# Optimization experiments

Hardware: AMD Instinct MI355X
Metric: run time of the kernel (lower is better)

Reference implementation:

```python
import jax, jax.numpy as jnp
import numpy as np
import math

D_EMB = 1024
N_HEADS = 16
D_HEAD = D_EMB // N_HEADS
D_FF = 4 * D_EMB
BATCH = 2
SEQ = 2048
EPS = 1e-6


def setup_inputs() -> dict:
    key = jax.random.key(0)
    ks = jax.random.split(key, 12)
    s = 0.02
    return {
        "x": jax.random.normal(ks[0], (BATCH, SEQ, D_EMB), jnp.float32),
        "wq": jax.random.normal(ks[1], (D_EMB, D_EMB), jnp.float32) * s,
        "wk": jax.random.normal(ks[2], (D_EMB, D_EMB), jnp.float32) * s,
        "wv": jax.random.normal(ks[3], (D_EMB, D_EMB), jnp.float32) * s,
        "wo": jax.random.normal(ks[4], (D_EMB, D_EMB), jnp.float32) * s,
        "bo": jnp.zeros((D_EMB,), jnp.float32),
        "w1": jax.random.normal(ks[5], (D_FF, D_EMB), jnp.float32) * s,
        "b1": jnp.zeros((D_FF,), jnp.float32),
        "w2": jax.random.normal(ks[6], (D_EMB, D_FF), jnp.float32) * s,
        "b2": jnp.zeros((D_EMB,), jnp.float32),
        "ln1_s": jnp.ones((D_EMB,), jnp.float32),
        "ln1_b": jnp.zeros((D_EMB,), jnp.float32),
        "ln2_s": jnp.ones((D_EMB,), jnp.float32),
        "ln2_b": jnp.zeros((D_EMB,), jnp.float32),
    }


def _layernorm(x, scale, shift):
    mean = jnp.mean(x, axis=-1, keepdims=True)
    var = jnp.mean(jnp.square(x - mean), axis=-1, keepdims=True)  # unbiased=False
    return scale * (x - mean) / jnp.sqrt(var + EPS) + shift


def _gelu_tanh(x):
    c = math.sqrt(2.0 / math.pi)
    return 0.5 * x * (1.0 + jnp.tanh(c * (x + 0.044715 * x * x * x)))


def _attention(x, wq, wk, wv, wo, bo):
    B, S, _ = x.shape
    q = (x @ wq.T).reshape(B, S, N_HEADS, D_HEAD).transpose(0, 2, 1, 3)
    k = (x @ wk.T).reshape(B, S, N_HEADS, D_HEAD).transpose(0, 2, 1, 3)
    v = (x @ wv.T).reshape(B, S, N_HEADS, D_HEAD).transpose(0, 2, 1, 3)
    scores = jnp.einsum("bhqd,bhkd->bhqk", q, k)
    causal = jnp.triu(jnp.ones((S, S), bool), k=1)
    scores = jnp.where(causal, -jnp.inf, scores)
    weights = jax.nn.softmax(scores / math.sqrt(D_HEAD), axis=-1)
    ctx = jnp.einsum("bhqk,bhkd->bhqd", weights, v)
    ctx = ctx.transpose(0, 2, 1, 3).reshape(B, S, D_EMB)
    return ctx @ wo.T + bo


def reference(x, wq, wk, wv, wo, bo, w1, b1, w2, b2, ln1_s, ln1_b, ln2_s, ln2_b):
    # pre-norm attention block (dropout in eval mode = identity)
    h = x + _attention(_layernorm(x, ln1_s, ln1_b), wq, wk, wv, wo, bo)
    # pre-norm MLP with tanh-approx GeLU
    y = _layernorm(h, ln2_s, ln2_b)
    y = _gelu_tanh(y @ w1.T + b1) @ w2.T + b2
    return h + y
```

## Files before the change

kernel.cpp:

```cpp
#include <hip/hip_runtime.h>
#include <math.h>

typedef unsigned short u16;
typedef __attribute__((ext_vector_type(8))) __bf16 bf16x8v;
typedef __attribute__((ext_vector_type(8))) unsigned short ushort8v;
typedef __attribute__((ext_vector_type(4))) unsigned short ushort4v;
typedef __attribute__((ext_vector_type(4))) float f32x4v;

#define D_EMBD 1024
#define NHEADS 16
#define DHEAD  64
#define DFF    4096
#define BATCHN 2
#define SEQL   2048
#define TOK    (BATCHN*SEQL)

#define EPI_BF16_GELU    2
#define EPI_BF16_QKV     3
#define EPI_BF16_PART    5

__device__ __forceinline__ float bf2f(u16 s) {
  return __builtin_bit_cast(float, (unsigned)s << 16);
}
__device__ __forceinline__ u16 f2bf(float f) {
  unsigned u = __builtin_bit_cast(unsigned, f);
  unsigned r = u + 0x7fffu + ((u >> 16) & 1u);
  return (u16)(r >> 16);
}
__device__ __forceinline__ u16 f2bf_trunc(float f) {
  return (u16)(__builtin_bit_cast(unsigned, f) >> 16);
}

#define GLOAD16(gp, lp)                                                        \
  __builtin_amdgcn_global_load_lds(                                            \
      (__attribute__((address_space(1))) void*)(void*)(gp),                    \
      (__attribute__((address_space(3))) void*)(void*)(lp), 16, 0, 0)

__global__ __launch_bounds__(256) void cvt_all_kernel(const float* __restrict__ wq,
                                                      const float* __restrict__ wk,
                                                      const float* __restrict__ wv,
                                                      const float* __restrict__ wo,
                                                      const float* __restrict__ w1,
                                                      const float* __restrict__ w2,
                                                      u16* __restrict__ wcat,
                                                      u16* __restrict__ wob,
                                                      u16* __restrict__ w1b,
                                                      u16* __restrict__ w2b) {
  int bid = blockIdx.x;
  const float* src;
  u16* dst;
  int loc;
  if (bid < 4096) {
    int seg = bid >> 10;
    loc = (bid & 1023) * 256 + threadIdx.x;
    src = (seg == 0) ? wq : (seg == 1) ? wk : (seg == 2) ? wv : wo;
    dst = (seg == 0) ? wcat : (seg == 1) ? wcat + 1048576
                            : (seg == 2) ? wcat + 2097152 : wob;
  } else if (bid < 8192) {
    loc = (bid - 4096) * 256 + threadIdx.x;
    src = w1; dst = w1b;
  } else {
    loc = (bid - 8192) * 256 + threadIdx.x;
    src = w2; dst = w2b;
  }
  float4 v = ((const float4*)src)[loc];
  ushort4 o;
  o.x = f2bf(v.x); o.y = f2bf(v.y); o.z = f2bf(v.z); o.w = f2bf(v.w);
  ((ushort4*)dst)[loc] = o;
}

__global__ __launch_bounds__(256) void ln_kernel(const float* __restrict__ x,
                                                 const float* __restrict__ sc,
                                                 const float* __restrict__ sh,
                                                 u16* __restrict__ out) {
  int row = blockIdx.x, tid = threadIdx.x;
  const float4* xr = (const float4*)(x + (size_t)row * D_EMBD);
  float4 v = xr[tid];
  float s  = (v.x + v.y) + (v.z + v.w);
  float s2 = (v.x * v.x + v.y * v.y) + (v.z * v.z + v.w * v.w);
#pragma unroll
  for (int off = 32; off; off >>= 1) {
    s  += __shfl_xor(s, off, 64);
    s2 += __shfl_xor(s2, off, 64);
  }
  __shared__ float rs[4], rs2[4];
  int wave = tid >> 6, lane = tid & 63;
  if (lane == 0) { rs[wave] = s; rs2[wave] = s2; }
  __syncthreads();
  s  = (rs[0] + rs[1]) + (rs[2] + rs[3]);
  s2 = (rs2[0] + rs2[1]) + (rs2[2] + rs2[3]);
  float mean = s * (1.f / 1024.f);
  float var  = s2 * (1.f / 1024.f) - mean * mean;
  float rstd = rsqrtf(var + 1e-6f);
  float4 scv = ((const float4*)sc)[tid];
  float4 shv = ((const float4*)sh)[tid];
  ushort4 o;
  o.x = f2bf((v.x - mean) * rstd * scv.x + shv.x);
  o.y = f2bf((v.y - mean) * rstd * scv.y + shv.y);
  o.z = f2bf((v.z - mean) * rstd * scv.z + shv.z);
  o.w = f2bf((v.w - mean) * rstd * scv.w + shv.w);
  ((ushort4*)(out + (size_t)row * D_EMBD))[tid] = o;
}

__global__ __launch_bounds__(256) void ln2f_kernel(const u16* __restrict__ parts,
                                                   const float* __restrict__ x,
                                                   const float* __restrict__ bo,
                                                   const float* __restrict__ sc,
                                                   const float* __restrict__ sh,
                                                   float* __restrict__ hbuf,
                                                   u16* __restrict__ ybuf) {
  int row = blockIdx.x, tid = threadIdx.x;
  size_t base4 = (size_t)row * 256 + tid;
  float4 v = ((const float4*)x)[base4];
  float4 bv = ((const float4*)bo)[tid];
  v.x += bv.x; v.y += bv.y; v.z += bv.z; v.w += bv.w;
#pragma unroll
  for (int p = 0; p < 4; ++p) {
    ushort4 u = ((const ushort4*)parts)[(size_t)p * 1048576 + base4];
    v.x += bf2f(u.x); v.y += bf2f(u.y); v.z += bf2f(u.z); v.w += bf2f(u.w);
  }
  ((float4*)hbuf)[base4] = v;
  float s  = (v.x + v.y) + (v.z + v.w);
  float s2 = (v.x * v.x + v.y * v.y) + (v.z * v.z + v.w * v.w);
#pragma unroll
  for (int off = 32; off; off >>= 1) {
    s  += __shfl_xor(s, off, 64);
    s2 += __shfl_xor(s2, off, 64);
  }
  __shared__ float rs[4], rs2[4];
  int wave = tid >> 6, lane = tid & 63;
  if (lane == 0) { rs[wave] = s; rs2[wave] = s2; }
  __syncthreads();
  s  = (rs[0] + rs[1]) + (rs[2] + rs[3]);
  s2 = (rs2[0] + rs2[1]) + (rs2[2] + rs2[3]);
  float mean = s * (1.f / 1024.f);
  float var  = s2 * (1.f / 1024.f) - mean * mean;
  float rstd = rsqrtf(var + 1e-6f);
  float4 scv = ((const float4*)sc)[tid];
  float4 shv = ((const float4*)sh)[tid];
  ushort4 o;
  o.x = f2bf((v.x - mean) * rstd * scv.x + shv.x);
  o.y = f2bf((v.y - mean) * rstd * scv.y + shv.y);
  o.z = f2bf((v.z - mean) * rstd * scv.z + shv.z);
  o.w = f2bf((v.w - mean) * rstd * scv.w + shv.w);
  ((ushort4*)ybuf)[base4] = o;
}

__global__ __launch_bounds__(256) void reduce_w2_kernel(const u16* __restrict__ parts,
                                                        const float* __restrict__ resid,
                                                        const float* __restrict__ bias,
                                                        float* __restrict__ out) {
  int i = blockIdx.x * 256 + threadIdx.x;
  float4 r = ((const float4*)resid)[i];
  float4 bi = ((const float4*)bias)[i & 255];
  float s0 = 0, s1 = 0, s2 = 0, s3 = 0;
#pragma unroll
  for (int p = 0; p < 4; ++p) {
    ushort4 u = ((const ushort4*)parts)[(size_t)p * 1048576 + i];
    s0 += bf2f(u.x); s1 += bf2f(u.y); s2 += bf2f(u.z); s3 += bf2f(u.w);
  }
  float4 o = {s0 + r.x + bi.x, s1 + r.y + bi.y, s2 + r.z + bi.z, s3 + r.w + bi.w};
  ((float4*)out)[i] = o;
}

template <int MH, int NH, bool READA, class FS, class FG>
__device__ __forceinline__ void gphase(const u16* sm, int cur, int wm, int wn,
                                       int lr, int quad,
                                       f32x4v (&acc)[8][4], bf16x8v (&av)[4][2],
                                       FS&& st, FG&& gate) {
  const int sx = lr & 7;
  bf16x8v bv[2][2];
  if constexpr (READA) {
#pragma unroll
    for (int j2 = 0; j2 < 4; ++j2) {
      int g = 2 * (MH * 4 + j2) + wm;
      int row = g * 16 + lr;
#pragma unroll
      for (int kk = 0; kk < 2; ++kk) {
        int slot = (kk * 4 + quad) ^ sx;
        av[j2][kk] = *(const bf16x8v*)(sm + cur * 32768 + row * 64 + slot * 8);
      }
    }
  }
#pragma unroll
  for (int i2 = 0; i2 < 2; ++i2) {
    int h = wn + 4 * (NH * 2 + i2);
    int row = h * 16 + lr;
#pragma unroll
    for (int kk = 0; kk < 2; ++kk) {
      int slot = (kk * 4 + quad) ^ sx;
      bv[i2][kk] = *(const bf16x8v*)(sm + cur * 32768 + 16384 + row * 64 + slot * 8);
    }
  }
  st();
  gate();
  __builtin_amdgcn_s_barrier();
  asm volatile("s_waitcnt lgkmcnt(0)" ::: "memory");
  __builtin_amdgcn_sched_barrier(0);
  __builtin_amdgcn_s_setprio(1);
#pragma unroll
  for (int j2 = 0; j2 < 4; ++j2)
#pragma unroll
    for (int i2 = 0; i2 < 2; ++i2)
#pragma unroll
      for (int kk = 0; kk < 2; ++kk)
        acc[MH * 4 + j2][NH * 2 + i2] = __builtin_amdgcn_mfma_f32_16x16x32_bf16(
            av[j2][kk], bv[i2][kk], acc[MH * 4 + j2][NH * 2 + i2], 0, 0, 0);
  __builtin_amdgcn_s_setprio(0);
  __builtin_amdgcn_sched_barrier(0);
  __builtin_amdgcn_s_barrier();
}

template <int EPI>
__global__ __launch_bounds__(512, 2) void gemm256(const u16* __restrict__ A,
                                                  const u16* __restrict__ W,
                                                  u16* __restrict__ Cb,
                                                  const float* __restrict__ bias,
                                                  int M, int N, int K) {
  __shared__ __align__(16) u16 sm[65536];
  const int tid = threadIdx.x;
  const int wave = tid >> 6, lane = tid & 63;
  const int lr = lane & 15, quad = lane >> 4;
  const int wm = wave >> 2, wn = wave & 3;
  const int m0 = blockIdx.y * 256, n0 = blockIdx.x * 256;
  const int KC = K / gridDim.z;
  const int kbeg = blockIdx.z * KC;
  const int NT = KC >> 6;
  const size_t poff = (size_t)blockIdx.z * ((size_t)M * N);

  const int r8 = lane >> 3;
  const int sslot = (lane & 7) ^ r8;
  const int rb0 = wave * 2;

  auto stA = [&](int bb, int h, int tk) {
#pragma unroll
    for (int s = 0; s < 2; ++s) {
      const u16* gp = A + (size_t)(m0 + h * 128 + (rb0 + s) * 8 + r8) * K +
                      (kbeg + tk * 64 + sslot * 8);
      GLOAD16(gp, (char*)sm + bb * 65536 + h * 16384 + (rb0 + s) * 1024);
    }
  };
  auto stB = [&](int bb, int h, int tk) {
#pragma unroll
    for (int s = 0; s < 2; ++s) {
      const u16* gp = W + (size_t)(n0 + h * 128 + (rb0 + s) * 8 + r8) * K +
                      (kbeg + tk * 64 + sslot * 8);
      GLOAD16(gp, (char*)sm + bb * 65536 + 32768 + h * 16384 + (rb0 + s) * 1024);
    }
  };

  f32x4v acc[8][4];
#pragma unroll
  for (int j = 0; j < 8; ++j)
#pragma unroll
    for (int i = 0; i < 4; ++i) {
      f32x4v z = {0.f, 0.f, 0.f, 0.f};
      acc[j][i] = z;
    }
  bf16x8v av[4][2];

  stA(0, 0, 0); stB(0, 0, 0); stA(0, 1, 0); stB(0, 1, 0);
  stA(1, 0, 1); stB(1, 1, 1);
  asm volatile("s_waitcnt vmcnt(4)" ::: "memory");
  __builtin_amdgcn_s_barrier();

  for (int t = 0; t < NT; ++t) {
    const int cur = t & 1, nb = cur ^ 1;
    const bool p1 = (t + 1 < NT), p2 = (t + 2 < NT);
    gphase<0, 0, true>(sm, cur, wm, wn, lr, quad, acc, av,
        [&] { if (p1) stB(nb, 0, t + 1); }, [&] {});
    gphase<0, 1, false>(sm, cur, wm, wn, lr, quad, acc, av,
        [&] { if (p1) stA(nb, 1, t + 1); }, [&] {});
    gphase<1, 1, true>(sm, cur, wm, wn, lr, quad, acc, av,
        [&] { if (p2) stA(cur, 0, t + 2); }, [&] {});
    gphase<1, 0, false>(sm, cur, wm, wn, lr, quad, acc, av,
        [&] { if (p2) stB(cur, 1, t + 2); },
        [&] {
          if (p2) { asm volatile("s_waitcnt vmcnt(4)" ::: "memory"); }
          else    { asm volatile("s_waitcnt vmcnt(0)" ::: "memory"); }
        });
  }

  const bool qsc = (EPI == EPI_BF16_QKV) && (n0 < 1024);
#pragma unroll
  for (int j = 0; j < 8; ++j) {
    int gr = m0 + (2 * j + wm) * 16 + quad * 4;
#pragma unroll
    for (int i = 0; i < 4; ++i) {
      int gc = n0 + (wn + 4 * i) * 16 + lr;
      float bi = 0.f;
      if constexpr (EPI == EPI_BF16_GELU) bi = bias[gc];
#pragma unroll
      for (int r = 0; r < 4; ++r) {
        size_t idx = (size_t)(gr + r) * N + gc;
        float v = acc[j][i][r];
        if constexpr (EPI == EPI_BF16_PART) {
          Cb[poff + idx] = f2bf(v);
        } else if constexpr (EPI == EPI_BF16_QKV) {
          Cb[idx] = f2bf(qsc ? v * 0.125f : v);
        } else {
          v += bi;
          float z = 0.7978845608028654f * (v + 0.044715f * v * v * v);
          float tt = 2.f / (1.f + __expf(-2.f * z)) - 1.f;
          Cb[idx] = f2bf(0.5f * v * (1.f + tt));
        }
      }
    }
  }
}

#define VTS 72
__device__ __forceinline__ void stage_k8(const u16* Kbase, int ks, u16* kfbuf,
                                         int wave, int lr, int quad) {
  int key = ((wave >> 1) << 4) + lr;
  int c8 = ((wave & 1) << 2) + quad;
  GLOAD16(Kbase + (size_t)(ks + key) * 3072 + c8 * 8, (char*)kfbuf + wave * 1024);
}
__device__ __forceinline__ void load_v(const u16* Vbase, int ks, int vkey0, int vc8,
                                       ushort8v& va, ushort8v& vb) {
  va = *(const ushort8v*)(Vbase + (size_t)(ks + vkey0) * 3072 + vc8 * 8);
  vb = *(const ushort8v*)(Vbase + (size_t)(ks + vkey0 + 1) * 3072 + vc8 * 8);
}
__device__ __forceinline__ void write_vt(u16* vt, int vc8, int vcol,
                                         ushort8v va, ushort8v vb) {
#pragma unroll
  for (int j = 0; j < 8; ++j) {
    unsigned pk = (unsigned)va[j] | ((unsigned)vb[j] << 16);
    *(unsigned*)(vt + (size_t)(vc8 * 8 + j) * VTS + vcol) = pk;
  }
}

__global__ __launch_bounds__(512) void attn_kernel(const u16* __restrict__ qkv,
                                                   u16* __restrict__ ctx) {
  __shared__ u16 Kf[2][4096];
  __shared__ u16 Vt[2][64 * VTS];
  int tid = threadIdx.x;
  int wave = tid >> 6, lane = tid & 63;
  int lr = lane & 15, quad = lane >> 4;
  int id = blockIdx.x;
  int bh = id & 31;
  int t = 15 - (id >> 5);
  int b = bh >> 4, h = bh & 15;
  int q0 = t * 128;
  const u16* qkvb = qkv + (size_t)(b * SEQL) * 3072;
  int qrow = q0 + wave * 16 + lr;
  const u16* Qp = qkvb + (size_t)qrow * 3072 + h * 64 + quad * 8;
  bf16x8v qf0 = *(const bf16x8v*)(Qp);
  bf16x8v qf1 = *(const bf16x8v*)(Qp + 32);
  const u16* Kbase = qkvb + 1024 + h * 64;
  const u16* Vbase = qkvb + 2048 + h * 64;
  const bool vstager = (tid < 256);
  int vkey0 = ((tid & 255) >> 3) * 2, vc8 = tid & 7;
  int vcol = vkey0 ^ (vc8 << 2);

  float m = -INFINITY, l = 0.f;
  f32x4v accO[4];
#pragma unroll
  for (int r = 0; r < 4; r++) {
    f32x4v z = {0.f, 0.f, 0.f, 0.f};
    accO[r] = z;
  }

  int nkt = 2 * t + 2;
  {
    stage_k8(Kbase, 0, Kf[0], wave, lr, quad);
    if (vstager) {
      ushort8v va, vb;
      load_v(Vbase, 0, vkey0, vc8, va, vb);
      write_vt(Vt[0], vc8, vcol, va, vb);
    }
  }
  __syncthreads();

  for (int kt = 0; kt < nkt; ++kt) {
    int cur = kt & 1, nxt = cur ^ 1;
    ushort8v va, vb;
    bool pre = (kt + 1 < nkt);
    if (pre) {
      stage_k8(Kbase, (kt + 1) * 64, Kf[nxt], wave, lr, quad);
      if (vstager) load_v(Vbase, (kt + 1) * 64, vkey0, vc8, va, vb);
    }
    bool active = !(kt == 2 * t + 1 && wave < 4);
    if (active) {
      const bf16x8v* Kc = (const bf16x8v*)Kf[cur];
      const u16* Vc = Vt[cur];
      f32x4v accS[4];
#pragma unroll
      for (int jb = 0; jb < 4; jb++) {
        f32x4v z = {0.f, 0.f, 0.f, 0.f};
        accS[jb] = z;
      }
#pragma unroll
      for (int jb = 0; jb < 4; jb++) {
        accS[jb] = __builtin_amdgcn_mfma_f32_16x16x32_bf16(Kc[((jb * 2 + 0) << 6) + lane], qf0, accS[jb], 0, 0, 0);
        accS[jb] = __builtin_amdgcn_mfma_f32_16x16x32_bf16(Kc[((jb * 2 + 1) << 6) + lane], qf1, accS[jb], 0, 0, 0);
      }
      if (kt >= 2 * t) {
        int kb = (kt - 2 * t) << 6;
#pragma unroll
        for (int jb = 0; jb < 4; jb++)
#pragma unroll
          for (int r = 0; r < 4; r++)
            if (kb + jb * 16 + quad * 4 + r > wave * 16 + lr) accS[jb][r] = -INFINITY;
      }
      float smax = accS[0][0];
#pragma unroll
      for (int jb = 0; jb < 4; jb++)
#pragma unroll
        for (int r = 0; r < 4; r++) smax = fmaxf(smax, accS[jb][r]);
      smax = fmaxf(smax, __shfl_xor(smax, 16, 64));
      smax = fmaxf(smax, __shfl_xor(smax, 32, 64));
      float mn = fmaxf(m, smax);
      float alpha = __expf(m - mn);
      m = mn;
      float ps = 0.f;
#pragma unroll
      for (int jb = 0; jb < 4; jb++)
#pragma unroll
        for (int r = 0; r < 4; r++) {
          accS[jb][r] = __expf(accS[jb][r] - mn);
          ps += accS[jb][r];
        }
      ps += __shfl_xor(ps, 16, 64);
      ps += __shfl_xor(ps, 32, 64);
      l = l * alpha + ps;
      float ar[4];
#pragma unroll
      for (int r = 0; r < 4; r++) ar[r] = __shfl(alpha, quad * 4 + r, 16);
#pragma unroll
      for (int nb = 0; nb < 4; nb++)
#pragma unroll
        for (int r = 0; r < 4; r++) accO[nb][r] *= ar[r];
#pragma unroll
      for (int kk = 0; kk < 2; ++kk) {
        ushort8v pp;
#pragma unroll
        for (int j = 0; j < 4; ++j) {
          pp[j]     = f2bf_trunc(accS[2 * kk][j]);
          pp[j + 4] = f2bf_trunc(accS[2 * kk + 1][j]);
        }
        bf16x8v pav = __builtin_bit_cast(bf16x8v, pp);
#pragma unroll
        for (int nb = 0; nb < 4; nb++) {
          int dim = nb * 16 + lr;
          int f = (nb * 2 + (lr >> 3)) & 7;
          int col1 = (kk * 32 + quad * 4) ^ (f << 2);
          ushort4v v0 = *(const ushort4v*)(Vc + dim * VTS + col1);
          ushort4v v1 = *(const ushort4v*)(Vc + dim * VTS + (col1 ^ 16));
          ushort8v vv;
#pragma unroll
          for (int j = 0; j < 4; ++j) { vv[j] = v0[j]; vv[j + 4] = v1[j]; }
          accO[nb] = __builtin_amdgcn_mfma_f32_16x16x32_bf16(pav, __builtin_bit_cast(bf16x8v, vv), accO[nb], 0, 0, 0);
        }
      }
    }
    if (pre && vstager) write_vt(Vt[nxt], vc8, vcol, va, vb);
    __syncthreads();
  }
  float linv = 1.f / l;
  float rr[4];
#pragma unroll
  for (int r = 0; r < 4; r++) rr[r] = __shfl(linv, quad * 4 + r, 16);
#pragma unroll
  for (int nb = 0; nb < 4; nb++)
#pragma unroll
    for (int r = 0; r < 4; r++) {
      int rowg = q0 + wave * 16 + quad * 4 + r;
      ctx[(size_t)(b * SEQL + rowg) * D_EMBD + h * 64 + nb * 16 + lr] =
          f2bf(accO[nb][r] * rr[r]);
    }
}

extern "C" void kernel_launch(void* const* d_in, const int* in_sizes, int n_in,
                              void* d_out, int out_size, void* d_ws, size_t ws_size,
                              hipStream_t stream) {
  const float* x    = (const float*)d_in[0];
  const float* wq   = (const float*)d_in[1];
  const float* wk   = (const float*)d_in[2];
  const float* wv   = (const float*)d_in[3];
  const float* wo   = (const float*)d_in[4];
  const float* bo   = (const float*)d_in[5];
  const float* w1   = (const float*)d_in[6];
  const float* b1   = (const float*)d_in[7];
  const float* w2   = (const float*)d_in[8];
  const float* b2   = (const float*)d_in[9];
  const float* ln1s = (const float*)d_in[10];
  const float* ln1b = (const float*)d_in[11];
  const float* ln2s = (const float*)d_in[12];
  const float* ln2b = (const float*)d_in[13];
  float* out = (float*)d_out;

  char* base = (char*)d_ws;
  size_t off = 0;
  auto alloc = [&](size_t bytes) {
    char* r = base + off;
    off += (bytes + 255) & ~(size_t)255;
    return r;
  };
  u16*   wcat = (u16*)alloc((size_t)3072 * 1024 * 2);
  u16*   wob  = (u16*)alloc((size_t)1024 * 1024 * 2);
  u16*   w1b  = (u16*)alloc((size_t)4096 * 1024 * 2);
  u16*   w2b  = (u16*)alloc((size_t)1024 * 4096 * 2);
  u16*   xn   = (u16*)alloc((size_t)TOK * 1024 * 2);
  u16*   qkv  = (u16*)alloc((size_t)TOK * 3072 * 2);
  u16*   ctx  = (u16*)alloc((size_t)TOK * 1024 * 2);
  float* hbuf = (float*)alloc((size_t)TOK * 1024 * 4);
  u16*   ybuf = (u16*)alloc((size_t)TOK * 1024 * 2);
  u16*   gbuf = (u16*)alloc((size_t)TOK * 4096 * 2);
  u16* woP = (u16*)xn;
  u16* w2P = (u16*)xn;

  cvt_all_kernel<<<12288, 256, 0, stream>>>(wq, wk, wv, wo, w1, w2,
                                            wcat, wob, w1b, w2b);
  ln_kernel<<<TOK, 256, 0, stream>>>(x, ln1s, ln1b, xn);
  gemm256<EPI_BF16_QKV><<<dim3(12, 16), 512, 0, stream>>>(
      xn, wcat, qkv, nullptr, TOK, 3072, 1024);
  attn_kernel<<<512, 512, 0, stream>>>(qkv, ctx);
  gemm256<EPI_BF16_PART><<<dim3(4, 16, 4), 512, 0, stream>>>(
      ctx, wob, woP, nullptr, TOK, 1024, 1024);
  ln2f_kernel<<<TOK, 256, 0, stream>>>(woP, x, bo, ln2s, ln2b, hbuf, ybuf);
  gemm256<EPI_BF16_GELU><<<dim3(16, 16), 512, 0, stream>>>(
      ybuf, w1b, gbuf, b1, TOK, 4096, 1024);
  gemm256<EPI_BF16_PART><<<dim3(4, 16, 4), 512, 0, stream>>>(
      gbuf, w2b, w2P, nullptr, TOK, 1024, 4096);
  reduce_w2_kernel<<<4096, 256, 0, stream>>>(w2P, hbuf, b2, out);
}
```

Baseline: 339.4 us.

## Swizzle GEMM block order across XCDs and reuse B fragments across phases

```diff
diff --git a/kernel.cpp b/kernel.cpp
--- a/kernel.cpp
+++ b/kernel.cpp
@@ -163,53 +163,9 @@
   ((float4*)out)[i] = o;
 }
 
-template <int MH, int NH, bool READA, class FS, class FG>
-__device__ __forceinline__ void gphase(const u16* sm, int cur, int wm, int wn,
-                                       int lr, int quad,
-                                       f32x4v (&acc)[8][4], bf16x8v (&av)[4][2],
-                                       FS&& st, FG&& gate) {
-  const int sx = lr & 7;
-  bf16x8v bv[2][2];
-  if constexpr (READA) {
-#pragma unroll
-    for (int j2 = 0; j2 < 4; ++j2) {
-      int g = 2 * (MH * 4 + j2) + wm;
-      int row = g * 16 + lr;
-#pragma unroll
-      for (int kk = 0; kk < 2; ++kk) {
-        int slot = (kk * 4 + quad) ^ sx;
-        av[j2][kk] = *(const bf16x8v*)(sm + cur * 32768 + row * 64 + slot * 8);
-      }
-    }
-  }
-#pragma unroll
-  for (int i2 = 0; i2 < 2; ++i2) {
-    int h = wn + 4 * (NH * 2 + i2);
-    int row = h * 16 + lr;
-#pragma unroll
-    for (int kk = 0; kk < 2; ++kk) {
-      int slot = (kk * 4 + quad) ^ sx;
-      bv[i2][kk] = *(const bf16x8v*)(sm + cur * 32768 + 16384 + row * 64 + slot * 8);
-    }
-  }
-  st();
-  gate();
-  __builtin_amdgcn_s_barrier();
-  asm volatile("s_waitcnt lgkmcnt(0)" ::: "memory");
-  __builtin_amdgcn_sched_barrier(0);
-  __builtin_amdgcn_s_setprio(1);
-#pragma unroll
-  for (int j2 = 0; j2 < 4; ++j2)
-#pragma unroll
-    for (int i2 = 0; i2 < 2; ++i2)
-#pragma unroll
-      for (int kk = 0; kk < 2; ++kk)
-        acc[MH * 4 + j2][NH * 2 + i2] = __builtin_amdgcn_mfma_f32_16x16x32_bf16(
-            av[j2][kk], bv[i2][kk], acc[MH * 4 + j2][NH * 2 + i2], 0, 0, 0);
-  __builtin_amdgcn_s_setprio(0);
-  __builtin_amdgcn_sched_barrier(0);
-  __builtin_amdgcn_s_barrier();
-}
+#define GBAR  __builtin_amdgcn_s_barrier()
+#define LGKM0 do { asm volatile("s_waitcnt lgkmcnt(0)" ::: "memory"); \
+                   __builtin_amdgcn_sched_barrier(0); } while (0)
 
 template <int EPI>
 __global__ __launch_bounds__(512, 2) void gemm256(const u16* __restrict__ A,
@@ -222,15 +178,23 @@
   const int wave = tid >> 6, lane = tid & 63;
   const int lr = lane & 15, quad = lane >> 4;
   const int wm = wave >> 2, wn = wave & 3;
-  const int m0 = blockIdx.y * 256, n0 = blockIdx.x * 256;
+  const int gx = gridDim.x, gy = gridDim.y;
+  const int nwg = gx * gy * gridDim.z;
+  const int bid = blockIdx.x + gx * (blockIdx.y + gy * blockIdx.z);
+  const int swz = (bid & 7) * (nwg >> 3) + (bid >> 3);
+  const int bx = swz % gx;
+  const int r1 = swz / gx;
+  const int by = r1 % gy, bz = r1 / gy;
+  const int m0 = by * 256, n0 = bx * 256;
   const int KC = K / gridDim.z;
-  const int kbeg = blockIdx.z * KC;
+  const int kbeg = bz * KC;
   const int NT = KC >> 6;
-  const size_t poff = (size_t)blockIdx.z * ((size_t)M * N);
+  const size_t poff = (size_t)bz * ((size_t)M * N);
 
   const int r8 = lane >> 3;
   const int sslot = (lane & 7) ^ r8;
   const int rb0 = wave * 2;
+  const int sx = lr & 7;
 
   auto stA = [&](int bb, int h, int tk) {
 #pragma unroll
@@ -248,6 +212,28 @@
       GLOAD16(gp, (char*)sm + bb * 65536 + 32768 + h * 16384 + (rb0 + s) * 1024);
     }
   };
+  auto ldA = [&](bf16x8v (&av)[4][2], int mh, int cur) {
+#pragma unroll
+    for (int j2 = 0; j2 < 4; ++j2) {
+      int row = (2 * (mh * 4 + j2) + wm) * 16 + lr;
+#pragma unroll
+      for (int kk = 0; kk < 2; ++kk) {
+        int slot = (kk * 4 + quad) ^ sx;
+        av[j2][kk] = *(const bf16x8v*)(sm + cur * 32768 + row * 64 + slot * 8);
+      }
+    }
+  };
+  auto ldB = [&](bf16x8v (&bv)[2][2], int nh, int cur) {
+#pragma unroll
+    for (int i2 = 0; i2 < 2; ++i2) {
+      int row = (wn + 4 * (nh * 2 + i2)) * 16 + lr;
+#pragma unroll
+      for (int kk = 0; kk < 2; ++kk) {
+        int slot = (kk * 4 + quad) ^ sx;
+        bv[i2][kk] = *(const bf16x8v*)(sm + cur * 32768 + 16384 + row * 64 + slot * 8);
+      }
+    }
+  };
 
   f32x4v acc[8][4];
 #pragma unroll
@@ -257,28 +243,46 @@
       f32x4v z = {0.f, 0.f, 0.f, 0.f};
       acc[j][i] = z;
     }
-  bf16x8v av[4][2];
+  bf16x8v av[4][2], bv0[2][2], bv1[2][2];
+
+  auto MMA = [&](int mh, int nh, bf16x8v (&a)[4][2], bf16x8v (&b)[2][2]) {
+    GBAR;
+    LGKM0;
+    __builtin_amdgcn_s_setprio(1);
+#pragma unroll
+    for (int j2 = 0; j2 < 4; ++j2)
+#pragma unroll
+      for (int i2 = 0; i2 < 2; ++i2)
+#pragma unroll
+        for (int kk = 0; kk < 2; ++kk)
+          acc[mh * 4 + j2][nh * 2 + i2] = __builtin_amdgcn_mfma_f32_16x16x32_bf16(
+              a[j2][kk], b[i2][kk], acc[mh * 4 + j2][nh * 2 + i2], 0, 0, 0);
+    __builtin_amdgcn_s_setprio(0);
+    __builtin_amdgcn_sched_barrier(0);
+    GBAR;
+  };
 
   stA(0, 0, 0); stB(0, 0, 0); stA(0, 1, 0); stB(0, 1, 0);
   stA(1, 0, 1); stB(1, 1, 1);
   asm volatile("s_waitcnt vmcnt(4)" ::: "memory");
-  __builtin_amdgcn_s_barrier();
+  GBAR;
 
   for (int t = 0; t < NT; ++t) {
     const int cur = t & 1, nb = cur ^ 1;
     const bool p1 = (t + 1 < NT), p2 = (t + 2 < NT);
-    gphase<0, 0, true>(sm, cur, wm, wn, lr, quad, acc, av,
-        [&] { if (p1) stB(nb, 0, t + 1); }, [&] {});
-    gphase<0, 1, false>(sm, cur, wm, wn, lr, quad, acc, av,
-        [&] { if (p1) stA(nb, 1, t + 1); }, [&] {});
-    gphase<1, 1, true>(sm, cur, wm, wn, lr, quad, acc, av,
-        [&] { if (p2) stA(cur, 0, t + 2); }, [&] {});
-    gphase<1, 0, false>(sm, cur, wm, wn, lr, quad, acc, av,
-        [&] { if (p2) stB(cur, 1, t + 2); },
-        [&] {
-          if (p2) { asm volatile("s_waitcnt vmcnt(4)" ::: "memory"); }
-          else    { asm volatile("s_waitcnt vmcnt(0)" ::: "memory"); }
-        });
+    ldA(av, 0, cur); ldB(bv0, 0, cur);
+    if (p1) stB(nb, 0, t + 1);
+    MMA(0, 0, av, bv0);
+    ldB(bv1, 1, cur);
+    if (p1) stA(nb, 1, t + 1);
+    MMA(0, 1, av, bv1);
+    ldA(av, 1, cur);
+    if (p2) stA(cur, 0, t + 2);
+    MMA(1, 1, av, bv1);
+    if (p2) stB(cur, 1, t + 2);
+    if (p2) { asm volatile("s_waitcnt vmcnt(4)" ::: "memory"); }
+    else    { asm volatile("s_waitcnt vmcnt(0)" ::: "memory"); }
+    MMA(1, 0, av, bv0);
   }
 
   const bool qsc = (EPI == EPI_BF16_QKV) && (n0 < 1024);
```

After: 334.6 us. No clear change (-1.4%).
